# Kernel optimization log

Measured on AMD Instinct MI355X. Metric: run time of the kernel, lower is better.

## Reference

```python
import jax, jax.numpy as jnp
import numpy as np

D_MODEL = 768
EXPAND = 2
D_INNER = EXPAND * D_MODEL  # 1536
D_STATE = 16
D_CONV = 4
DT_RANK = D_MODEL // 16  # 48
N_LAYER = 3
BATCH, SEQLEN = 2, 1024
EPS = 1e-5


def setup_inputs() -> dict:
    key = jax.random.key(0)
    ks = jax.random.split(key, 8)
    s = 0.02
    hidden_states = jax.random.normal(ks[0], (BATCH, SEQLEN, D_MODEL), jnp.float32)
    norm_w = jnp.ones((N_LAYER, D_MODEL), jnp.float32)
    in_proj_w = s * jax.random.normal(ks[1], (N_LAYER, 2 * D_INNER, D_MODEL), jnp.float32)
    conv_w = s * jax.random.normal(ks[2], (N_LAYER, D_INNER, D_CONV), jnp.float32)
    conv_b = jnp.zeros((N_LAYER, D_INNER), jnp.float32)
    x_proj_w = s * jax.random.normal(ks[3], (N_LAYER, DT_RANK + 2 * D_STATE, D_INNER), jnp.float32)
    dt_proj_w = s * jax.random.normal(ks[4], (N_LAYER, D_INNER, DT_RANK), jnp.float32)
    dt_proj_b = jnp.full((N_LAYER, D_INNER), -4.6, jnp.float32)  # softplus ~ 0.01
    # S4D-real init: A_log = log(1..d_state), tiled over channels
    A_log = jnp.tile(jnp.log(jnp.arange(1, D_STATE + 1, dtype=jnp.float32))[None, None, :], (N_LAYER, D_INNER, 1))
    D_skip = jnp.ones((N_LAYER, D_INNER), jnp.float32)
    out_proj_w = s * jax.random.normal(ks[5], (N_LAYER, D_MODEL, D_INNER), jnp.float32)
    norm_f_w = jnp.ones((D_MODEL,), jnp.float32)
    return dict(hidden_states=hidden_states, norm_w=norm_w, in_proj_w=in_proj_w,
                conv_w=conv_w, conv_b=conv_b, x_proj_w=x_proj_w, dt_proj_w=dt_proj_w,
                dt_proj_b=dt_proj_b, A_log=A_log, D_skip=D_skip, out_proj_w=out_proj_w,
                norm_f_w=norm_f_w)


def _rmsnorm(x, w):
    return x * jax.lax.rsqrt(jnp.mean(x * x, axis=-1, keepdims=True) + EPS) * w


def _causal_conv1d(x, w, b):
    # x: [B, L, D]; w: [D, K] depthwise; left-pad for causality
    xt = jnp.transpose(x, (0, 2, 1))  # [B, D, L]
    y = jax.lax.conv_general_dilated(xt, w[:, None, :], window_strides=(1,),
                                     padding=[(D_CONV - 1, 0)], feature_group_count=D_INNER)
    return jnp.transpose(y, (0, 2, 1)) + b


def _selective_scan(u, delta, A, Bc, Cc, Dp):
    # u, delta: [B, L, D]; A: [D, N]; Bc, Cc: [B, L, N]
    def step(h, inp):
        dt, bt, ct, ut = inp  # [B,D], [B,N], [B,N], [B,D]
        h = jnp.exp(dt[..., None] * A) * h + (dt * ut)[..., None] * bt[:, None, :]
        y = jnp.einsum('bdn,bn->bd', h, ct)
        return h, y
    h0 = jnp.zeros((u.shape[0], u.shape[2], A.shape[1]), u.dtype)
    xs = (jnp.swapaxes(delta, 0, 1), jnp.swapaxes(Bc, 0, 1), jnp.swapaxes(Cc, 0, 1), jnp.swapaxes(u, 0, 1))
    _, ys = jax.lax.scan(step, h0, xs)  # ys: [L, B, D]
    return jnp.swapaxes(ys, 0, 1) + u * Dp


def _mixer(h, in_w, cw, cb, xw, dtw, dtb, A_log, Dp, ow):
    xz = jnp.einsum('bld,ed->ble', h, in_w)  # [B, L, 2*D_INNER]
    x, z = xz[..., :D_INNER], xz[..., D_INNER:]
    x = jax.nn.silu(_causal_conv1d(x, cw, cb))
    x_dbl = jnp.einsum('bld,ed->ble', x, xw)
    dt = x_dbl[..., :DT_RANK]
    Bc = x_dbl[..., DT_RANK:DT_RANK + D_STATE]
    Cc = x_dbl[..., DT_RANK + D_STATE:]
    delta = jax.nn.softplus(jnp.einsum('blr,dr->bld', dt, dtw) + dtb)
    A = -jnp.exp(A_log)
    y = _selective_scan(x, delta, A, Bc, Cc, Dp)
    y = y * jax.nn.silu(z)
    return jnp.einsum('bld,ed->ble', y, ow)


def reference(hidden_states, norm_w, in_proj_w, conv_w, conv_b, x_proj_w, dt_proj_w,
              dt_proj_b, A_log, D_skip, out_proj_w, norm_f_w):
    hidden = hidden_states
    residual = None
    for i in range(N_LAYER):
        residual = hidden if residual is None else hidden + residual  # fused add
        hidden = _rmsnorm(residual, norm_w[i])
        hidden = _mixer(hidden, in_proj_w[i], conv_w[i], conv_b[i], x_proj_w[i],
                        dt_proj_w[i], dt_proj_b[i], A_log[i], D_skip[i], out_proj_w[i])
    # final fused add + RMSNorm (prenorm=False)
    return _rmsnorm(hidden + residual, norm_f_w)
```

## Files before the change

### kernel.cpp

```cpp
#include <hip/hip_runtime.h>
#include <math.h>

#define D_MODEL 768
#define D_INNER 1536
#define D_STATE 16
#define D_CONV 4
#define DT_RANK 48
#define N_LAYER 3
#define BATCH 2
#define SEQLEN 1024
#define NROWS (BATCH * SEQLEN)
#define XDBL_W (DT_RANK + 2 * D_STATE)
#define EPS 1e-5f

#define SCLEN 16
#define SDN 16

typedef short bf16x8 __attribute__((ext_vector_type(8)));
typedef float f32x4 __attribute__((ext_vector_type(4)));

__device__ __forceinline__ ushort f2bf(float x) {
    union { float f; uint u; } v; v.f = x;
    uint r = v.u + 0x7fff + ((v.u >> 16) & 1);
    return (ushort)(r >> 16);
}
__device__ __forceinline__ float bf2f(ushort x) {
    union { uint u; float f; } v; v.u = ((uint)x) << 16;
    return v.f;
}

__device__ __forceinline__ void gload_lds16(const void* g, void* l) {
    __builtin_amdgcn_global_load_lds(
        (const __attribute__((address_space(1))) unsigned int*)g,
        (__attribute__((address_space(3))) unsigned int*)l, 16, 0, 0);
}

#define CVT_N0 (3 * 3072 * 768 / 4)
#define CVT_N1 (3 * 768 * 1536 / 4)
#define CVT_N2 (3 * 128 * 1536 / 4)
#define CVT_N3 (3 * 1536 * 64 / 4)
#define CVT_C1 (CVT_N0)
#define CVT_C2 (CVT_C1 + CVT_N1)
#define CVT_C3 (CVT_C2 + CVT_N2)
#define CVT_TOT (CVT_C3 + CVT_N3)

__global__ __launch_bounds__(256) void cvt_all_kernel(
    const float* __restrict__ w_in, const float* __restrict__ w_out,
    const float* __restrict__ w_x, const float* __restrict__ w_dt,
    ushort* __restrict__ d_in, ushort* __restrict__ d_out,
    ushort* __restrict__ d_x, ushort* __restrict__ d_dt)
{
    int i = blockIdx.x * 256 + threadIdx.x;
    if (i < CVT_C1) {
        float4 v = ((const float4*)w_in)[i];
        ushort4 o; o.x = f2bf(v.x); o.y = f2bf(v.y); o.z = f2bf(v.z); o.w = f2bf(v.w);
        ((ushort4*)d_in)[i] = o;
    } else if (i < CVT_C2) {
        int j = i - CVT_C1;
        float4 v = ((const float4*)w_out)[j];
        ushort4 o; o.x = f2bf(v.x); o.y = f2bf(v.y); o.z = f2bf(v.z); o.w = f2bf(v.w);
        ((ushort4*)d_out)[j] = o;
    } else if (i < CVT_C3) {
        int j = i - CVT_C2;
        const int per = 128 * 1536 / 4;
        int li = j / per, rem = j - li * per;
        int r = (rem * 4) / 1536, c = (rem * 4) % 1536;
        ushort4 o = make_ushort4(0, 0, 0, 0);
        if (r < XDBL_W) {
            const float* s = w_x + ((size_t)li * XDBL_W + r) * 1536 + c;
            o.x = f2bf(s[0]); o.y = f2bf(s[1]); o.z = f2bf(s[2]); o.w = f2bf(s[3]);
        }
        ((ushort4*)d_x)[j] = o;
    } else if (i < CVT_TOT) {
        int j = i - CVT_C3;
        const int per = 1536 * 64 / 4;
        int li = j / per, rem = j - li * per;
        int r = (rem * 4) / 64, c = (rem * 4) % 64;
        ushort4 o = make_ushort4(0, 0, 0, 0);
        if (c < DT_RANK) {
            const float* s = w_dt + ((size_t)li * 1536 + r) * DT_RANK + c;
            o.x = f2bf(s[0]); o.y = f2bf(s[1]); o.z = f2bf(s[2]); o.w = f2bf(s[3]);
        }
        ((ushort4*)d_dt)[j] = o;
    }
}

__global__ __launch_bounds__(256) void add_rmsnorm_kernel(
    const float* __restrict__ x, const float* __restrict__ res_in,
    const float* __restrict__ w, float* __restrict__ res_out,
    float* __restrict__ normed_f32, ushort* __restrict__ normed_bf)
{
    int row = blockIdx.x;
    int tid = threadIdx.x;
    const float* xr = x + row * D_MODEL;
    float v[3];
    float ss = 0.f;
#pragma unroll
    for (int i = 0; i < 3; i++) {
        int c = tid + i * 256;
        float t = xr[c];
        if (res_in) t += res_in[row * D_MODEL + c];
        v[i] = t;
        ss += t * t;
    }
    for (int off = 32; off; off >>= 1) ss += __shfl_xor(ss, off, 64);
    __shared__ float red[4];
    if ((tid & 63) == 0) red[tid >> 6] = ss;
    __syncthreads();
    float tot = red[0] + red[1] + red[2] + red[3];
    float scale = rsqrtf(tot * (1.f / D_MODEL) + EPS);
#pragma unroll
    for (int i = 0; i < 3; i++) {
        int c = tid + i * 256;
        if (res_out) res_out[row * D_MODEL + c] = v[i];
        float o = v[i] * scale * w[c];
        if (normed_f32) normed_f32[row * D_MODEL + c] = o;
        if (normed_bf)  normed_bf[row * D_MODEL + c] = f2bf(o);
    }
}

template <int BM, int BN, int EPI, int OUTBF>
__global__ __launch_bounds__(256) void gemm_mfma_kernel(
    const ushort* __restrict__ A, const ushort* __restrict__ W,
    const float* __restrict__ bias, void* __restrict__ Cv,
    ushort* __restrict__ C2, int ldc, int Nout, int M, int K)
{
    constexpr int TM = BM / 32;
    constexpr int TN = BN / 32;
    __shared__ __attribute__((aligned(16))) ushort As[BM * 64];
    __shared__ __attribute__((aligned(16))) ushort Ws[BN * 64];
    const int t = threadIdx.x;
    const int lane = t & 63, w = t >> 6;
    const int ln15 = lane & 15, q = lane >> 4;
    const int row0 = blockIdx.y * BM, col0 = blockIdx.x * BN;
    const int wm0 = (w & 1) * (BM / 2), wn0 = (w >> 1) * (BN / 2);

    float* Cf = (float*)Cv;
    ushort* Cb = (ushort*)Cv;

    f32x4 acc[TM][TN];
#pragma unroll
    for (int i = 0; i < TM; i++)
#pragma unroll
        for (int j = 0; j < TN; j++) acc[i][j] = (f32x4){0.f, 0.f, 0.f, 0.f};

    for (int k0 = 0; k0 < K; k0 += 64) {
        __syncthreads();
#pragma unroll
        for (int i = 0; i < BM / 32; i++) {
            int p = (i * 4 + w) * 64 + lane;
            int r = p >> 3, s = p & 7;
            int g = s ^ (r & 7);
            gload_lds16(A + (size_t)(row0 + r) * K + k0 + g * 8, &As[p * 8]);
        }
#pragma unroll
        for (int i = 0; i < BN / 32; i++) {
            int p = (i * 4 + w) * 64 + lane;
            int r = p >> 3, s = p & 7;
            int g = s ^ (r & 7);
            gload_lds16(W + (size_t)(col0 + r) * K + k0 + g * 8, &Ws[p * 8]);
        }
        __syncthreads();
#pragma unroll
        for (int ks = 0; ks < 2; ks++) {
            bf16x8 af[TM], wf[TN];
#pragma unroll
            for (int im = 0; im < TM; im++) {
                int m = wm0 + im * 16 + ln15;
                int slot = (ks * 4 + q) ^ (m & 7);
                af[im] = *(const bf16x8*)&As[m * 64 + slot * 8];
            }
#pragma unroll
            for (int jn = 0; jn < TN; jn++) {
                int n = wn0 + jn * 16 + ln15;
                int slot = (ks * 4 + q) ^ (n & 7);
                wf[jn] = *(const bf16x8*)&Ws[n * 64 + slot * 8];
            }
#pragma unroll
            for (int im = 0; im < TM; im++)
#pragma unroll
                for (int jn = 0; jn < TN; jn++)
                    acc[im][jn] = __builtin_amdgcn_mfma_f32_16x16x32_bf16(
                        af[im], wf[jn], acc[im][jn], 0, 0, 0);
        }
    }
#pragma unroll
    for (int im = 0; im < TM; im++) {
#pragma unroll
        for (int jn = 0; jn < TN; jn++) {
            int rr = row0 + wm0 + im * 16 + q * 4;
            int cc = col0 + wn0 + jn * 16 + ln15;
#pragma unroll
            for (int r = 0; r < 4; r++) {
                float v = acc[im][jn][r];
                if (EPI == 2) {
                    if (cc < Nout) Cf[(size_t)(rr + r) * ldc + cc] = v;
                    if (cc < DT_RANK)  C2[(size_t)(rr + r) * 64 + cc] = f2bf(v);
                    else if (cc < 64)  C2[(size_t)(rr + r) * 64 + cc] = 0;
                } else if (cc < Nout) {
                    if (EPI == 1) {
                        v += bias[cc];
                        v = (v > 20.f) ? v : log1pf(__expf(v));
                    }
                    if (OUTBF) Cb[(size_t)(rr + r) * ldc + cc] = f2bf(v);
                    else       Cf[(size_t)(rr + r) * ldc + cc] = v;
                }
            }
        }
    }
}

__global__ __launch_bounds__(256) void conv_silu_kernel(
    const ushort* __restrict__ xzbf, const float* __restrict__ cw,
    const float* __restrict__ cb, ushort* __restrict__ out_bf)
{
    int idx = blockIdx.x * 256 + threadIdx.x;
    int d = idx % D_INNER;
    int bl = idx / D_INNER;
    int l = bl % SEQLEN;
    float s = cb[d];
    const ushort* xp = xzbf + (size_t)bl * (2 * D_INNER) + d;
#pragma unroll
    for (int k = 0; k < D_CONV; k++) {
        int ls = l - (D_CONV - 1) + k;
        if (ls >= 0) s += cw[d * D_CONV + k] * bf2f(xp[(k - (D_CONV - 1)) * (2 * D_INNER)]);
    }
    float sil = s / (1.f + __expf(-s));
    out_bf[(size_t)bl * D_INNER + d] = f2bf(sil);
}

__global__ __launch_bounds__(1024) void scan2_kernel(
    const ushort* __restrict__ ubf, const float* __restrict__ delta,
    const float* __restrict__ A_log, const float* __restrict__ xdbl,
    const float* __restrict__ Dskip, const ushort* __restrict__ xzbf,
    ushort* __restrict__ ybf)
{
    __shared__ float PL[16][SDN * 17];
    __shared__ float HL[16][SDN * 17];
    const int t = threadIdx.x;
    const int lane = t & 63;
    const int w = t >> 6;
    const int dsub = lane & 15;
    const int csub = lane >> 4;
    const int c = w * 4 + csub;
    const int b = blockIdx.x / (D_INNER / SDN);
    const int d = (blockIdx.x % (D_INNER / SDN)) * SDN + dsub;

    float a2[D_STATE];
#pragma unroll
    for (int n = 0; n < D_STATE; n++)
        a2[n] = -__expf(A_log[d * D_STATE + n]) * 1.44269504f;

    const size_t base = (size_t)b * SEQLEN * D_INNER + d;
    const float* dtp = delta + base;
    const ushort* up = ubf + base;
    const float* xrow = xdbl + (size_t)b * SEQLEN * XDBL_W;
    const int l0 = c * SCLEN;

    float h[D_STATE], P[D_STATE];
#pragma unroll
    for (int n = 0; n < D_STATE; n++) { h[n] = 0.f; P[n] = 1.f; }

    for (int i = 0; i < SCLEN; i++) {
        const int l = l0 + i;
        float dt = dtp[(size_t)l * D_INNER];
        float uu = bf2f(up[(size_t)l * D_INNER]);
        const float4* Bv = (const float4*)(xrow + (size_t)l * XDBL_W + DT_RANK);
        float4 q0 = Bv[0], q1 = Bv[1], q2 = Bv[2], q3 = Bv[3];
        float Bf[D_STATE] = {q0.x,q0.y,q0.z,q0.w, q1.x,q1.y,q1.z,q1.w,
                             q2.x,q2.y,q2.z,q2.w, q3.x,q3.y,q3.z,q3.w};
        float dtu = dt * uu;
#pragma unroll
        for (int n = 0; n < D_STATE; n++) {
            float e = __builtin_amdgcn_exp2f(dt * a2[n]);
            P[n] *= e;
            h[n] = e * h[n] + dtu * Bf[n];
        }
    }

#pragma unroll
    for (int n = 0; n < D_STATE; n++) {
        float Pp = __shfl(P[n], lane - 16, 64);
        float Hp = __shfl(h[n], lane - 16, 64);
        bool act = csub >= 1;
        h[n] = act ? P[n] * Hp + h[n] : h[n];
        P[n] = act ? P[n] * Pp : P[n];
    }
#pragma unroll
    for (int n = 0; n < D_STATE; n++) {
        float Pp = __shfl(P[n], lane - 32, 64);
        float Hp = __shfl(h[n], lane - 32, 64);
        bool act = csub >= 2;
        h[n] = act ? P[n] * Hp + h[n] : h[n];
        P[n] = act ? P[n] * Pp : P[n];
    }

    if (csub == 3) {
#pragma unroll
        for (int n = 0; n < D_STATE; n++) {
            PL[w][dsub * 17 + n] = P[n];
            HL[w][dsub * 17 + n] = h[n];
        }
    }
    __syncthreads();

    if (t < SDN * D_STATE) {
        const int d2 = t >> 4, n2 = t & 15;
        float hin = 0.f;
        for (int ww = 0; ww < 16; ww++) {
            float Pw = PL[ww][d2 * 17 + n2];
            float Hw = HL[ww][d2 * 17 + n2];
            HL[ww][d2 * 17 + n2] = hin;
            hin = Pw * hin + Hw;
        }
    }
    __syncthreads();

#pragma unroll
    for (int n = 0; n < D_STATE; n++) {
        float Win = HL[w][dsub * 17 + n];
        float Pe = __shfl(P[n], lane - 16, 64);
        float He = __shfl(h[n], lane - 16, 64);
        h[n] = (csub == 0) ? Win : Pe * Win + He;
    }

    const float Dsk = Dskip[d];
    const ushort* zp = xzbf + (size_t)b * SEQLEN * (2 * D_INNER) + D_INNER + d;
    ushort* yp = ybf + base;
    for (int i = 0; i < SCLEN; i++) {
        const int l = l0 + i;
        float dt = dtp[(size_t)l * D_INNER];
        float uu = bf2f(up[(size_t)l * D_INNER]);
        float zz = bf2f(zp[(size_t)l * (2 * D_INNER)]);
        const float4* Bv = (const float4*)(xrow + (size_t)l * XDBL_W + DT_RANK);
        float4 q0 = Bv[0], q1 = Bv[1], q2 = Bv[2], q3 = Bv[3];
        float4 r0 = Bv[4], r1 = Bv[5], r2 = Bv[6], r3 = Bv[7];
        float Bf[D_STATE] = {q0.x,q0.y,q0.z,q0.w, q1.x,q1.y,q1.z,q1.w,
                             q2.x,q2.y,q2.z,q2.w, q3.x,q3.y,q3.z,q3.w};
        float Cf[D_STATE] = {r0.x,r0.y,r0.z,r0.w, r1.x,r1.y,r1.z,r1.w,
                             r2.x,r2.y,r2.z,r2.w, r3.x,r3.y,r3.z,r3.w};
        float dtu = dt * uu;
        float acc = 0.f;
#pragma unroll
        for (int n = 0; n < D_STATE; n++) {
            float e = __builtin_amdgcn_exp2f(dt * a2[n]);
            h[n] = e * h[n] + dtu * Bf[n];
            acc += h[n] * Cf[n];
        }
        float yy = acc + uu * Dsk;
        float ee = __builtin_amdgcn_exp2f(-zz * 1.44269504f);
        float sil = zz * __builtin_amdgcn_rcpf(1.f + ee);
        yp[(size_t)l * D_INNER] = f2bf(yy * sil);
    }
}

extern "C" void kernel_launch(void* const* d_in, const int* in_sizes, int n_in,
                              void* d_out, int out_size, void* d_ws, size_t ws_size,
                              hipStream_t stream)
{
    const float* hs        = (const float*)d_in[0];
    const float* norm_w    = (const float*)d_in[1];
    const float* in_proj_w = (const float*)d_in[2];
    const float* conv_w    = (const float*)d_in[3];
    const float* conv_b    = (const float*)d_in[4];
    const float* x_proj_w  = (const float*)d_in[5];
    const float* dt_proj_w = (const float*)d_in[6];
    const float* dt_proj_b = (const float*)d_in[7];
    const float* A_log     = (const float*)d_in[8];
    const float* D_skip    = (const float*)d_in[9];
    const float* out_proj_w= (const float*)d_in[10];
    const float* norm_f_w  = (const float*)d_in[11];

    float* ws = (float*)d_ws;
    float* residual = ws;
    float* hidden   = residual + NROWS * D_MODEL;
    float* xdbl     = hidden + NROWS * D_MODEL;
    float* delta    = xdbl + NROWS * XDBL_W;
    ushort* xzbf    = (ushort*)(delta + NROWS * D_INNER);
    ushort* normbf  = xzbf + (size_t)NROWS * 2 * D_INNER;
    ushort* ybf     = normbf + NROWS * D_MODEL;
    ushort* xconvbf = ybf + NROWS * D_INNER;
    ushort* xdtbf   = xconvbf + NROWS * D_INNER;
    ushort* win_bf  = xdtbf + NROWS * 64;
    ushort* wout_bf = win_bf + (size_t)N_LAYER * 2 * D_INNER * D_MODEL;
    ushort* xw_pad  = wout_bf + (size_t)N_LAYER * D_MODEL * D_INNER;
    ushort* dtw_pad = xw_pad + (size_t)N_LAYER * 128 * 1536;

    cvt_all_kernel<<<(CVT_TOT + 255) / 256, 256, 0, stream>>>(
        in_proj_w, out_proj_w, x_proj_w, dt_proj_w,
        win_bf, wout_bf, xw_pad, dtw_pad);

    for (int i = 0; i < N_LAYER; i++) {
        add_rmsnorm_kernel<<<NROWS, 256, 0, stream>>>(
            i == 0 ? hs : hidden, i == 0 ? nullptr : residual,
            norm_w + i * D_MODEL, residual, nullptr, normbf);
        gemm_mfma_kernel<64, 128, 0, 1><<<dim3(2 * D_INNER / 128, NROWS / 64), 256, 0, stream>>>(
            normbf, win_bf + (size_t)i * 2 * D_INNER * D_MODEL, nullptr,
            xzbf, nullptr, 2 * D_INNER, 2 * D_INNER, NROWS, D_MODEL);
        conv_silu_kernel<<<NROWS * D_INNER / 256, 256, 0, stream>>>(
            xzbf, conv_w + i * D_INNER * D_CONV, conv_b + i * D_INNER, xconvbf);
        gemm_mfma_kernel<32, 128, 2, 0><<<dim3(1, NROWS / 32), 256, 0, stream>>>(
            xconvbf, xw_pad + (size_t)i * 128 * 1536, nullptr,
            xdbl, xdtbf, XDBL_W, XDBL_W, NROWS, D_INNER);
        gemm_mfma_kernel<64, 128, 1, 0><<<dim3(D_INNER / 128, NROWS / 64), 256, 0, stream>>>(
            xdtbf, dtw_pad + (size_t)i * 1536 * 64, dt_proj_b + i * D_INNER,
            delta, nullptr, D_INNER, D_INNER, NROWS, 64);
        scan2_kernel<<<BATCH * (D_INNER / SDN), 1024, 0, stream>>>(
            xconvbf, delta, A_log + (size_t)i * D_INNER * D_STATE, xdbl,
            D_skip + i * D_INNER, xzbf, ybf);
        gemm_mfma_kernel<64, 64, 0, 0><<<dim3(D_MODEL / 64, NROWS / 64), 256, 0, stream>>>(
            ybf, wout_bf + (size_t)i * D_MODEL * D_INNER, nullptr,
            hidden, nullptr, D_MODEL, D_MODEL, NROWS, D_INNER);
    }
    add_rmsnorm_kernel<<<NROWS, 256, 0, stream>>>(
        hidden, residual, norm_f_w, nullptr, (float*)d_out, nullptr);
}
```

Before: 501.9 us.

## Fuse causal conv+SiLU into x_proj GEMM and scan, drop conv buffer

Removes the standalone conv_silu kernel and its bf16 intermediate buffer. The x_proj GEMM now computes the depthwise conv and SiLU on the fly from a 35-row halo tile of xz staged in shared memory, and the scan recomputes the conv output per timestep from a sliding window of three previous inputs. The in_proj GEMM tile also grows from 64x128 to 128x128. This trades a launch and a full write plus read of the conv output for redundant conv arithmetic in two kernels and strided reads of the wider xz buffer.

```diff
diff --git a/kernel.cpp b/kernel.cpp
--- a/kernel.cpp
+++ b/kernel.cpp
@@ -123,7 +123,7 @@
 __global__ __launch_bounds__(256) void gemm_mfma_kernel(
     const ushort* __restrict__ A, const ushort* __restrict__ W,
     const float* __restrict__ bias, void* __restrict__ Cv,
-    ushort* __restrict__ C2, int ldc, int Nout, int M, int K)
+    int ldc, int Nout, int M, int K)
 {
     constexpr int TM = BM / 32;
     constexpr int TN = BN / 32;
@@ -190,14 +190,10 @@
         for (int jn = 0; jn < TN; jn++) {
             int rr = row0 + wm0 + im * 16 + q * 4;
             int cc = col0 + wn0 + jn * 16 + ln15;
-#pragma unroll
-            for (int r = 0; r < 4; r++) {
-                float v = acc[im][jn][r];
-                if (EPI == 2) {
-                    if (cc < Nout) Cf[(size_t)(rr + r) * ldc + cc] = v;
-                    if (cc < DT_RANK)  C2[(size_t)(rr + r) * 64 + cc] = f2bf(v);
-                    else if (cc < 64)  C2[(size_t)(rr + r) * 64 + cc] = 0;
-                } else if (cc < Nout) {
+            if (cc < Nout) {
+#pragma unroll
+                for (int r = 0; r < 4; r++) {
+                    float v = acc[im][jn][r];
                     if (EPI == 1) {
                         v += bias[cc];
                         v = (v > 20.f) ? v : log1pf(__expf(v));
@@ -210,30 +206,104 @@
     }
 }
 
-__global__ __launch_bounds__(256) void conv_silu_kernel(
-    const ushort* __restrict__ xzbf, const float* __restrict__ cw,
-    const float* __restrict__ cb, ushort* __restrict__ out_bf)
+__global__ __launch_bounds__(256) void xproj_conv_kernel(
+    const ushort* __restrict__ xzbf, const ushort* __restrict__ W,
+    const float* __restrict__ cw, const float* __restrict__ cb,
+    float* __restrict__ xdbl, ushort* __restrict__ xdt)
 {
-    int idx = blockIdx.x * 256 + threadIdx.x;
-    int d = idx % D_INNER;
-    int bl = idx / D_INNER;
-    int l = bl % SEQLEN;
-    float s = cb[d];
-    const ushort* xp = xzbf + (size_t)bl * (2 * D_INNER) + d;
-#pragma unroll
-    for (int k = 0; k < D_CONV; k++) {
-        int ls = l - (D_CONV - 1) + k;
-        if (ls >= 0) s += cw[d * D_CONV + k] * bf2f(xp[(k - (D_CONV - 1)) * (2 * D_INNER)]);
-    }
-    float sil = s / (1.f + __expf(-s));
-    out_bf[(size_t)bl * D_INNER + d] = f2bf(sil);
+    __shared__ __attribute__((aligned(16))) ushort Xs[35 * 64];
+    __shared__ __attribute__((aligned(16))) ushort As[32 * 64];
+    __shared__ __attribute__((aligned(16))) ushort Ws[128 * 64];
+    __shared__ float cwS[64 * 4];
+    __shared__ float cbS[64];
+    const int t = threadIdx.x;
+    const int lane = t & 63, w = t >> 6;
+    const int ln15 = lane & 15, q = lane >> 4;
+    const int row0 = blockIdx.y * 32;
+    const bool halo_valid = (row0 & 1023) != 0;
+    const int wm0 = (w & 1) * 16, wn0 = (w >> 1) * 64;
+
+    f32x4 acc[4];
+#pragma unroll
+    for (int j = 0; j < 4; j++) acc[j] = (f32x4){0.f, 0.f, 0.f, 0.f};
+
+    for (int k0 = 0; k0 < D_INNER; k0 += 64) {
+        __syncthreads();
+        for (int it = t; it < 35 * 16; it += 256) {
+            int r = it >> 4, cq = it & 15;
+            int gr = row0 - 3 + r;
+            ushort4 v = make_ushort4(0, 0, 0, 0);
+            if (r >= 3 || halo_valid)
+                v = *(const ushort4*)&xzbf[(size_t)gr * (2 * D_INNER) + k0 + cq * 4];
+            *(ushort4*)&Xs[r * 64 + cq * 4] = v;
+        }
+        cwS[t] = cw[k0 * 4 + t];
+        if (t < 64) cbS[t] = cb[k0 + t];
+#pragma unroll
+        for (int i = 0; i < 4; i++) {
+            int p = (i * 4 + w) * 64 + lane;
+            int r = p >> 3, s = p & 7;
+            int g = s ^ (r & 7);
+            gload_lds16(W + (size_t)r * D_INNER + k0 + g * 8, &Ws[p * 8]);
+        }
+        __syncthreads();
+        {
+            int r = t >> 3, g = t & 7;
+            ushort out[8];
+#pragma unroll
+            for (int e = 0; e < 8; e++) {
+                int col = g * 8 + e;
+                float s = cbS[col];
+                s += cwS[col * 4 + 0] * bf2f(Xs[(r + 0) * 64 + col]);
+                s += cwS[col * 4 + 1] * bf2f(Xs[(r + 1) * 64 + col]);
+                s += cwS[col * 4 + 2] * bf2f(Xs[(r + 2) * 64 + col]);
+                s += cwS[col * 4 + 3] * bf2f(Xs[(r + 3) * 64 + col]);
+                float sil = s / (1.f + __expf(-s));
+                out[e] = f2bf(sil);
+            }
+            int slot = g ^ (r & 7);
+            *(bf16x8*)&As[r * 64 + slot * 8] = *(bf16x8*)out;
+        }
+        __syncthreads();
+#pragma unroll
+        for (int ks = 0; ks < 2; ks++) {
+            bf16x8 af, wf[4];
+            {
+                int m = wm0 + ln15;
+                int slot = (ks * 4 + q) ^ (m & 7);
+                af = *(const bf16x8*)&As[m * 64 + slot * 8];
+            }
+#pragma unroll
+            for (int jn = 0; jn < 4; jn++) {
+                int n = wn0 + jn * 16 + ln15;
+                int slot = (ks * 4 + q) ^ (n & 7);
+                wf[jn] = *(const bf16x8*)&Ws[n * 64 + slot * 8];
+            }
+#pragma unroll
+            for (int jn = 0; jn < 4; jn++)
+                acc[jn] = __builtin_amdgcn_mfma_f32_16x16x32_bf16(
+                    af, wf[jn], acc[jn], 0, 0, 0);
+        }
+    }
+#pragma unroll
+    for (int jn = 0; jn < 4; jn++) {
+        int rr = row0 + wm0 + q * 4;
+        int cc = wn0 + jn * 16 + ln15;
+#pragma unroll
+        for (int r = 0; r < 4; r++) {
+            float v = acc[jn][r];
+            if (cc < XDBL_W) xdbl[(size_t)(rr + r) * XDBL_W + cc] = v;
+            if (cc < DT_RANK)  xdt[(size_t)(rr + r) * 64 + cc] = f2bf(v);
+            else if (cc < 64)  xdt[(size_t)(rr + r) * 64 + cc] = 0;
+        }
+    }
 }
 
 __global__ __launch_bounds__(1024) void scan2_kernel(
-    const ushort* __restrict__ ubf, const float* __restrict__ delta,
+    const ushort* __restrict__ xzbf, const float* __restrict__ delta,
     const float* __restrict__ A_log, const float* __restrict__ xdbl,
-    const float* __restrict__ Dskip, const ushort* __restrict__ xzbf,
-    ushort* __restrict__ ybf)
+    const float* __restrict__ Dskip, const float* __restrict__ cw,
+    const float* __restrict__ cb, ushort* __restrict__ ybf)
 {
     __shared__ float PL[16][SDN * 17];
     __shared__ float HL[16][SDN * 17];
@@ -251,20 +321,35 @@
     for (int n = 0; n < D_STATE; n++)
         a2[n] = -__expf(A_log[d * D_STATE + n]) * 1.44269504f;
 
+    const float cw0 = cw[d * 4 + 0], cw1 = cw[d * 4 + 1];
+    const float cw2 = cw[d * 4 + 2], cw3 = cw[d * 4 + 3];
+    const float cbv = cb[d];
+
     const size_t base = (size_t)b * SEQLEN * D_INNER + d;
     const float* dtp = delta + base;
-    const ushort* up = ubf + base;
+    const ushort* xp = xzbf + (size_t)b * SEQLEN * (2 * D_INNER) + d;
+    const ushort* zp = xp + D_INNER;
     const float* xrow = xdbl + (size_t)b * SEQLEN * XDBL_W;
     const int l0 = c * SCLEN;
 
     float h[D_STATE], P[D_STATE];
 #pragma unroll
     for (int n = 0; n < D_STATE; n++) { h[n] = 0.f; P[n] = 1.f; }
+
+    float a3c = 0.f, a2c = 0.f, a1c = 0.f;
+    if (c > 0) {
+        a3c = bf2f(xp[(size_t)(l0 - 3) * (2 * D_INNER)]);
+        a2c = bf2f(xp[(size_t)(l0 - 2) * (2 * D_INNER)]);
+        a1c = bf2f(xp[(size_t)(l0 - 1) * (2 * D_INNER)]);
+    }
 
     for (int i = 0; i < SCLEN; i++) {
         const int l = l0 + i;
         float dt = dtp[(size_t)l * D_INNER];
-        float uu = bf2f(up[(size_t)l * D_INNER]);
+        float x0 = bf2f(xp[(size_t)l * (2 * D_INNER)]);
+        float s = cbv + cw0 * a3c + cw1 * a2c + cw2 * a1c + cw3 * x0;
+        a3c = a2c; a2c = a1c; a1c = x0;
+        float uu = s / (1.f + __expf(-s));
         const float4* Bv = (const float4*)(xrow + (size_t)l * XDBL_W + DT_RANK);
         float4 q0 = Bv[0], q1 = Bv[1], q2 = Bv[2], q3 = Bv[3];
         float Bf[D_STATE] = {q0.x,q0.y,q0.z,q0.w, q1.x,q1.y,q1.z,q1.w,
@@ -324,13 +409,21 @@
         h[n] = (csub == 0) ? Win : Pe * Win + He;
     }
 
+    a3c = 0.f; a2c = 0.f; a1c = 0.f;
+    if (c > 0) {
+        a3c = bf2f(xp[(size_t)(l0 - 3) * (2 * D_INNER)]);
+        a2c = bf2f(xp[(size_t)(l0 - 2) * (2 * D_INNER)]);
+        a1c = bf2f(xp[(size_t)(l0 - 1) * (2 * D_INNER)]);
+    }
     const float Dsk = Dskip[d];
-    const ushort* zp = xzbf + (size_t)b * SEQLEN * (2 * D_INNER) + D_INNER + d;
     ushort* yp = ybf + base;
     for (int i = 0; i < SCLEN; i++) {
         const int l = l0 + i;
         float dt = dtp[(size_t)l * D_INNER];
-        float uu = bf2f(up[(size_t)l * D_INNER]);
+        float x0 = bf2f(xp[(size_t)l * (2 * D_INNER)]);
+        float s = cbv + cw0 * a3c + cw1 * a2c + cw2 * a1c + cw3 * x0;
+        a3c = a2c; a2c = a1c; a1c = x0;
+        float uu = s / (1.f + __expf(-s));
         float zz = bf2f(zp[(size_t)l * (2 * D_INNER)]);
         const float4* Bv = (const float4*)(xrow + (size_t)l * XDBL_W + DT_RANK);
         float4 q0 = Bv[0], q1 = Bv[1], q2 = Bv[2], q3 = Bv[3];
@@ -379,8 +472,7 @@
     ushort* xzbf    = (ushort*)(delta + NROWS * D_INNER);
     ushort* normbf  = xzbf + (size_t)NROWS * 2 * D_INNER;
     ushort* ybf     = normbf + NROWS * D_MODEL;
-    ushort* xconvbf = ybf + NROWS * D_INNER;
-    ushort* xdtbf   = xconvbf + NROWS * D_INNER;
+    ushort* xdtbf   = ybf + NROWS * D_INNER;
     ushort* win_bf  = xdtbf + NROWS * 64;
     ushort* wout_bf = win_bf + (size_t)N_LAYER * 2 * D_INNER * D_MODEL;
     ushort* xw_pad  = wout_bf + (size_t)N_LAYER * D_MODEL * D_INNER;
@@ -394,23 +486,23 @@
         add_rmsnorm_kernel<<<NROWS, 256, 0, stream>>>(
             i == 0 ? hs : hidden, i == 0 ? nullptr : residual,
             norm_w + i * D_MODEL, residual, nullptr, normbf);
-        gemm_mfma_kernel<64, 128, 0, 1><<<dim3(2 * D_INNER / 128, NROWS / 64), 256, 0, stream>>>(
+        gemm_mfma_kernel<128, 128, 0, 1><<<dim3(2 * D_INNER / 128, NROWS / 128), 256, 0, stream>>>(
             normbf, win_bf + (size_t)i * 2 * D_INNER * D_MODEL, nullptr,
-            xzbf, nullptr, 2 * D_INNER, 2 * D_INNER, NROWS, D_MODEL);
-        conv_silu_kernel<<<NROWS * D_INNER / 256, 256, 0, stream>>>(
-            xzbf, conv_w + i * D_INNER * D_CONV, conv_b + i * D_INNER, xconvbf);
-        gemm_mfma_kernel<32, 128, 2, 0><<<dim3(1, NROWS / 32), 256, 0, stream>>>(
-            xconvbf, xw_pad + (size_t)i * 128 * 1536, nullptr,
-            xdbl, xdtbf, XDBL_W, XDBL_W, NROWS, D_INNER);
+            xzbf, 2 * D_INNER, 2 * D_INNER, NROWS, D_MODEL);
+        xproj_conv_kernel<<<dim3(1, NROWS / 32), 256, 0, stream>>>(
+            xzbf, xw_pad + (size_t)i * 128 * 1536,
+            conv_w + i * D_INNER * D_CONV, conv_b + i * D_INNER,
+            xdbl, xdtbf);
         gemm_mfma_kernel<64, 128, 1, 0><<<dim3(D_INNER / 128, NROWS / 64), 256, 0, stream>>>(
             xdtbf, dtw_pad + (size_t)i * 1536 * 64, dt_proj_b + i * D_INNER,
-            delta, nullptr, D_INNER, D_INNER, NROWS, 64);
+            delta, D_INNER, D_INNER, NROWS, 64);
         scan2_kernel<<<BATCH * (D_INNER / SDN), 1024, 0, stream>>>(
-            xconvbf, delta, A_log + (size_t)i * D_INNER * D_STATE, xdbl,
-            D_skip + i * D_INNER, xzbf, ybf);
+            xzbf, delta, A_log + (size_t)i * D_INNER * D_STATE, xdbl,
+            D_skip + i * D_INNER, conv_w + i * D_INNER * D_CONV,
+            conv_b + i * D_INNER, ybf);
         gemm_mfma_kernel<64, 64, 0, 0><<<dim3(D_MODEL / 64, NROWS / 64), 256, 0, stream>>>(
             ybf, wout_bf + (size_t)i * D_MODEL * D_INNER, nullptr,
-            hidden, nullptr, D_MODEL, D_MODEL, NROWS, D_INNER);
+            hidden, D_MODEL, D_MODEL, NROWS, D_INNER);
     }
     add_rmsnorm_kernel<<<NROWS, 256, 0, stream>>>(
         hidden, residual, norm_f_w, nullptr, (float*)d_out, nullptr);
```

New measurement: 625.7 us. 24.6% more time.
